# Kernel optimization log

Measured on AMD Instinct MI355X. Metric: run time of the kernel, lower is better.

Reference implementation:

```python
import jax, jax.numpy as jnp
import numpy as np

HIDDEN = 2048
N_HEADS = 16
N_KV = 8
HEAD_DIM = HIDDEN // N_HEADS  # 128
EPS = 1e-6


def rms_norm(x, w, eps=EPS):
    xf = x.astype(jnp.float32)
    var = jnp.mean(xf * xf, axis=-1, keepdims=True)
    return (w * (xf * jax.lax.rsqrt(var + eps)).astype(x.dtype))


def rotate_half(x):
    x1, x2 = jnp.split(x, 2, axis=-1)
    return jnp.concatenate([-x2, x1], axis=-1)


def setup_inputs() -> dict:
    key = jax.random.key(0)
    ks = jax.random.split(key, 8)
    B, S = 2, 2048
    inp = {
        "hidden_states": jax.random.normal(ks[0], (B, S, HIDDEN), jnp.float32),
        "cos": jax.random.uniform(ks[1], (B, S, HEAD_DIM), jnp.float32, -1.0, 1.0),
        "sin": jax.random.uniform(ks[2], (B, S, HEAD_DIM), jnp.float32, -1.0, 1.0),
        "Wq": jax.random.normal(ks[3], (N_HEADS * HEAD_DIM, HIDDEN), jnp.float32) * 0.02,
        "Wk": jax.random.normal(ks[4], (N_KV * HEAD_DIM, HIDDEN), jnp.float32) * 0.02,
        "Wv": jax.random.normal(ks[5], (N_KV * HEAD_DIM, HIDDEN), jnp.float32) * 0.02,
        "Wo": jax.random.normal(ks[6], (HIDDEN, N_HEADS * HEAD_DIM), jnp.float32) * 0.02,
        "q_norm_w": jnp.ones((HEAD_DIM,), jnp.float32),
        "k_norm_w": jnp.ones((HEAD_DIM,), jnp.float32),
    }
    return inp


def reference(hidden_states, cos, sin, Wq, Wk, Wv, Wo, q_norm_w, k_norm_w):
    B, S, _ = hidden_states.shape
    scale = HEAD_DIM ** -0.5
    n_rep = N_HEADS // N_KV

    q = (hidden_states @ Wq.T).reshape(B, S, N_HEADS, HEAD_DIM)
    k = (hidden_states @ Wk.T).reshape(B, S, N_KV, HEAD_DIM)
    v = (hidden_states @ Wv.T).reshape(B, S, N_KV, HEAD_DIM)

    q = rms_norm(q, q_norm_w)
    k = rms_norm(k, k_norm_w)

    # -> (B, H, S, D)
    q = q.transpose(0, 2, 1, 3)
    k = k.transpose(0, 2, 1, 3)
    v = v.transpose(0, 2, 1, 3)

    c = cos[:, None, :, :]  # (B,1,S,D)
    s = sin[:, None, :, :]
    q = q * c + rotate_half(q) * s
    k = k * c + rotate_half(k) * s

    k = jnp.repeat(k, n_rep, axis=1)
    v = jnp.repeat(v, n_rep, axis=1)

    scores = jnp.einsum("bhqd,bhkd->bhqk", q, k) * scale
    attn = jax.nn.softmax(scores.astype(jnp.float32), axis=-1).astype(hidden_states.dtype)
    out = jnp.einsum("bhqk,bhkd->bhqd", attn, v)
    out = out.transpose(0, 2, 1, 3).reshape(B, S, N_HEADS * HEAD_DIM)
    return out @ Wo.T
```

## Files before the change

kernel.cpp:

```cpp
#include <hip/hip_runtime.h>
#include <cstdint>

#define SEQ 2048
#define BATCH 2
#define TOK 4096
#define HID 2048
#define NH 16
#define NKV 8
#define HD 128
#define QKV_LD 4096

using f16x8 = __attribute__((ext_vector_type(8))) _Float16;
using f32x4 = __attribute__((ext_vector_type(4))) float;

#define MFMA(a, b, c) __builtin_amdgcn_mfma_f32_16x16x32_f16(a, b, c, 0, 0, 0)

__device__ inline void gload16(const void* g, void* l) {
    __builtin_amdgcn_global_load_lds(
        (const __attribute__((address_space(1))) unsigned*)g,
        (__attribute__((address_space(3))) unsigned*)l, 16, 0, 0);
}

__device__ inline float exp2_fast(float x) {
#if __has_builtin(__builtin_amdgcn_exp2f)
    return __builtin_amdgcn_exp2f(x);
#else
    float r;
    asm("v_exp_f32 %0, %1\n\ts_nop 1" : "=v"(r) : "v"(x));
    return r;
#endif
}

__device__ inline unsigned cvt_pk2(float a, float b) {
    auto h = __builtin_amdgcn_cvt_pkrtz(a, b);
    return __builtin_bit_cast(unsigned, h);
}

__global__ __launch_bounds__(256) void conv_all(
    const float* __restrict__ hidden, const float* __restrict__ Wq,
    const float* __restrict__ Wk, const float* __restrict__ Wv,
    const float* __restrict__ Wo, _Float16* __restrict__ HhG,
    _Float16* __restrict__ WallH, _Float16* __restrict__ WoH)
{
    const int bid = blockIdx.x;
    const float* src;
    _Float16* dst;
    int row;
    if (bid < 4096)      { row = bid;        src = hidden; dst = HhG; }
    else if (bid < 6144) { row = bid - 4096; src = Wq;     dst = WallH; }
    else if (bid < 7168) { row = bid - 6144; src = Wk;     dst = WallH + (size_t)2048 * HID; }
    else if (bid < 8192) { row = bid - 7168; src = Wv;     dst = WallH + (size_t)3072 * HID; }
    else                 { row = bid - 8192; src = Wo;     dst = WoH; }

    const int gch = threadIdx.x;
    const float* s = src + (size_t)row * HID + gch * 8;
    float4 a = *(const float4*)s;
    float4 b = *(const float4*)(s + 4);
    f16x8 v;
    v[0] = (_Float16)a.x; v[1] = (_Float16)a.y;
    v[2] = (_Float16)a.z; v[3] = (_Float16)a.w;
    v[4] = (_Float16)b.x; v[5] = (_Float16)b.y;
    v[6] = (_Float16)b.z; v[7] = (_Float16)b.w;
    *(f16x8*)((char*)dst + (size_t)row * 4096 + gch * 16) = v;
}

template<bool HALF_OUT>
__global__ __launch_bounds__(512, 2) void gemm256(
    const _Float16* __restrict__ Ag, const _Float16* __restrict__ Bg,
    void* __restrict__ Cv, int ldc, int K)
{
    __shared__ char lds[2][4][16384];

    const int tid = threadIdx.x;
    const int wv = tid >> 6, ln = tid & 63;
    const int wm = wv >> 2, wn = wv & 3;
    const int lr = ln & 15, lq = ln >> 4;
    const int bn = blockIdx.x, bm = blockIdx.y;

    f32x4 acc[8][4] = {};

    const size_t arow0 = (size_t)bm * 256;
    const size_t brow0 = (size_t)bn * 256;

    const int g = tid & 7;
    uint32_t offA[2][2], offB[2][2];
#pragma unroll
    for (int i = 0; i < 2; ++i) {
        const int row = (i * 512 + tid) >> 3;
        const uint32_t sw = (uint32_t)((g ^ (row & 7)) << 4);
        offA[0][i] = (uint32_t)((arow0 + row) * 4096) + sw;
        offA[1][i] = (uint32_t)((arow0 + 128 + row) * 4096) + sw;
        offB[0][i] = (uint32_t)((brow0 + row) * 4096) + sw;
        offB[1][i] = (uint32_t)((brow0 + 128 + row) * 4096) + sw;
    }
    const int dst0 = wv * 64 * 16;

    const int swz0 = ((lq ^ (lr & 7)) << 4);
    const int swz1 = (((4 + lq) ^ (lr & 7)) << 4);

#define STAGE_ALL(bufsel, t)                                                   \
    { _Pragma("unroll")                                                        \
      for (int i = 0; i < 2; ++i) {                                            \
        gload16((const char*)Ag + offA[0][i] + (size_t)(t) * 128,              \
                &lds[bufsel][0][i * 8192 + dst0]);                             \
        gload16((const char*)Ag + offA[1][i] + (size_t)(t) * 128,              \
                &lds[bufsel][1][i * 8192 + dst0]);                             \
        gload16((const char*)Bg + offB[0][i] + (size_t)(t) * 128,              \
                &lds[bufsel][2][i * 8192 + dst0]);                             \
        gload16((const char*)Bg + offB[1][i] + (size_t)(t) * 128,              \
                &lds[bufsel][3][i * 8192 + dst0]);                             \
      } }

    STAGE_ALL(0, 0);
    asm volatile("s_waitcnt vmcnt(0)" ::: "memory");
    __builtin_amdgcn_s_barrier();

    const int NT = K / 64;
    for (int t = 0; t < NT; ++t) {
        const int buf = t & 1;
        const char* Ab = &lds[buf][wm][0];
        const char* Bb = &lds[buf][2 + (wn >> 1)][(wn & 1) * 64 * 128];

        f16x8 bfr[4][2];
#pragma unroll
        for (int nj = 0; nj < 4; ++nj) {
            bfr[nj][0] = *(const f16x8*)(Bb + (nj * 16 + lr) * 128 + swz0);
            bfr[nj][1] = *(const f16x8*)(Bb + (nj * 16 + lr) * 128 + swz1);
        }

        if (t + 1 < NT) STAGE_ALL(buf ^ 1, t + 1);

        __builtin_amdgcn_s_setprio(1);
#pragma unroll
        for (int mi = 0; mi < 8; ++mi) {
            f16x8 a0 = *(const f16x8*)(Ab + (mi * 16 + lr) * 128 + swz0);
            f16x8 a1 = *(const f16x8*)(Ab + (mi * 16 + lr) * 128 + swz1);
#pragma unroll
            for (int nj = 0; nj < 4; ++nj) {
                acc[mi][nj] = MFMA(a0, bfr[nj][0], acc[mi][nj]);
                acc[mi][nj] = MFMA(a1, bfr[nj][1], acc[mi][nj]);
            }
        }
        __builtin_amdgcn_s_setprio(0);

        asm volatile("s_waitcnt vmcnt(0)" ::: "memory");
        __builtin_amdgcn_s_barrier();
    }
#undef STAGE_ALL

#pragma unroll
    for (int mi = 0; mi < 8; ++mi)
#pragma unroll
        for (int r = 0; r < 4; ++r) {
            const size_t rowoff =
                (size_t)(arow0 + wm * 128 + mi * 16 + lq * 4 + r) * ldc
                + brow0 + wn * 64 + lr;
            if constexpr (HALF_OUT) {
                _Float16* rowp = (_Float16*)Cv + rowoff;
#pragma unroll
                for (int nj = 0; nj < 4; ++nj)
                    rowp[nj * 16] = (_Float16)acc[mi][nj][r];
            } else {
                float* rowp = (float*)Cv + rowoff;
#pragma unroll
                for (int nj = 0; nj < 4; ++nj)
                    rowp[nj * 16] = acc[mi][nj][r];
            }
        }
}

__global__ __launch_bounds__(512, 1) void gemm256x128(
    const _Float16* __restrict__ Ag, const _Float16* __restrict__ Bg,
    float* __restrict__ C, int ldc, int K)
{
    __shared__ char lds[2][3][16384];

    const int tid = threadIdx.x;
    const int wv = tid >> 6, ln = tid & 63;
    const int wm = wv >> 1, wn = wv & 1;
    const int lr = ln & 15, lq = ln >> 4;
    const int bn = blockIdx.x, bm = blockIdx.y;

    f32x4 acc[4][4] = {};

    const size_t arow0 = (size_t)bm * 256;
    const size_t brow0 = (size_t)bn * 128;

    const int g = tid & 7;
    uint32_t offA[2][2], offB[2];
#pragma unroll
    for (int i = 0; i < 2; ++i) {
        const int row = (i * 512 + tid) >> 3;
        const uint32_t sw = (uint32_t)((g ^ (row & 7)) << 4);
        offA[0][i] = (uint32_t)((arow0 + row) * 4096) + sw;
        offA[1][i] = (uint32_t)((arow0 + 128 + row) * 4096) + sw;
        offB[i]    = (uint32_t)((brow0 + row) * 4096) + sw;
    }
    const int dst0 = wv * 64 * 16;

    const int swz0 = ((lq ^ (lr & 7)) << 4);
    const int swz1 = (((4 + lq) ^ (lr & 7)) << 4);

#define STAGE_ALL2(bufsel, t)                                                  \
    { _Pragma("unroll")                                                        \
      for (int i = 0; i < 2; ++i) {                                            \
        gload16((const char*)Ag + offA[0][i] + (size_t)(t) * 128,              \
                &lds[bufsel][0][i * 8192 + dst0]);                             \
        gload16((const char*)Ag + offA[1][i] + (size_t)(t) * 128,              \
                &lds[bufsel][1][i * 8192 + dst0]);                             \
        gload16((const char*)Bg + offB[i] + (size_t)(t) * 128,                 \
                &lds[bufsel][2][i * 8192 + dst0]);                             \
      } }

    STAGE_ALL2(0, 0);
    asm volatile("s_waitcnt vmcnt(0)" ::: "memory");
    __builtin_amdgcn_s_barrier();

    const int NT = K / 64;
    for (int t = 0; t < NT; ++t) {
        const int buf = t & 1;
        const char* Ab = &lds[buf][wm >> 1][(wm & 1) * 64 * 128];
        const char* Bb = &lds[buf][2][wn * 64 * 128];

        f16x8 bfr[4][2];
#pragma unroll
        for (int nj = 0; nj < 4; ++nj) {
            bfr[nj][0] = *(const f16x8*)(Bb + (nj * 16 + lr) * 128 + swz0);
            bfr[nj][1] = *(const f16x8*)(Bb + (nj * 16 + lr) * 128 + swz1);
        }

        if (t + 1 < NT) STAGE_ALL2(buf ^ 1, t + 1);

        __builtin_amdgcn_s_setprio(1);
#pragma unroll
        for (int mi = 0; mi < 4; ++mi) {
            f16x8 a0 = *(const f16x8*)(Ab + (mi * 16 + lr) * 128 + swz0);
            f16x8 a1 = *(const f16x8*)(Ab + (mi * 16 + lr) * 128 + swz1);
#pragma unroll
            for (int nj = 0; nj < 4; ++nj) {
                acc[mi][nj] = MFMA(a0, bfr[nj][0], acc[mi][nj]);
                acc[mi][nj] = MFMA(a1, bfr[nj][1], acc[mi][nj]);
            }
        }
        __builtin_amdgcn_s_setprio(0);

        asm volatile("s_waitcnt vmcnt(0)" ::: "memory");
        __builtin_amdgcn_s_barrier();
    }
#undef STAGE_ALL2

#pragma unroll
    for (int mi = 0; mi < 4; ++mi)
#pragma unroll
        for (int r = 0; r < 4; ++r) {
            float* rowp = C + (size_t)(arow0 + wm * 64 + mi * 16 + lq * 4 + r) * ldc
                          + brow0 + wn * 64 + lr;
#pragma unroll
            for (int nj = 0; nj < 4; ++nj)
                rowp[nj * 16] = acc[mi][nj][r];
        }
}

__global__ __launch_bounds__(256) void norm_rope(
    const _Float16* __restrict__ P, const float* __restrict__ cosb,
    const float* __restrict__ sinb, const float* __restrict__ qw,
    const float* __restrict__ kw, _Float16* __restrict__ QhG,
    _Float16* __restrict__ KhG)
{
    const int t    = blockIdx.y;
    const int wave = threadIdx.x >> 6;
    const int lane = threadIdx.x & 63;
    const int hid  = blockIdx.x * 4 + wave;
    const float QS = 0.08838834764831845f * 1.4426950408889634f;

    const _Float16* ptr;
    const float* w;
    if (hid < NH) { ptr = P + (size_t)t * QKV_LD + hid * HD;              w = qw; }
    else          { ptr = P + (size_t)t * QKV_LD + HID + (hid - NH) * HD; w = kw; }

    float x1 = (float)ptr[lane];
    float x2 = (float)ptr[lane + 64];
    float ss = x1 * x1 + x2 * x2;
#pragma unroll
    for (int off = 1; off < 64; off <<= 1) ss += __shfl_xor(ss, off);
    const float r = rsqrtf(ss * (1.f / 128.f) + 1e-6f);
    const float n1 = x1 * r * w[lane];
    const float n2 = x2 * r * w[lane + 64];

    const float* cp = cosb + (size_t)t * HD;
    const float* sp = sinb + (size_t)t * HD;
    const float o1 = n1 * cp[lane]      - n2 * sp[lane];
    const float o2 = n2 * cp[lane + 64] + n1 * sp[lane + 64];

    if (hid < NH) {
        _Float16* qrow = QhG + (size_t)t * HID + hid * HD;
        qrow[lane]      = (_Float16)(o1 * QS);
        qrow[lane + 64] = (_Float16)(o2 * QS);
    } else {
        const int b = t / SEQ, s = t % SEQ, kv = hid - NH;
        char* ph = (char*)KhG + ((size_t)(b * NKV + kv) * SEQ + s) * 256;
        const int s7 = s & 7;
        const int d1 = lane, d2 = lane + 64;
        *(_Float16*)(ph + (((d1 >> 3) ^ s7) << 4) + ((d1 & 7) << 1)) = (_Float16)o1;
        *(_Float16*)(ph + (((d2 >> 3) ^ s7) << 4) + ((d2 & 7) << 1)) = (_Float16)o2;
    }
}

__global__ __launch_bounds__(256) void conv_v(
    const _Float16* __restrict__ P, _Float16* __restrict__ VtG)
{
    __shared__ _Float16 Ts[64][136];
    const int kb = blockIdx.x;
    const int kv = blockIdx.y;
    const int tid = threadIdx.x;

#pragma unroll
    for (int r = 0; r < 4; ++r) {
        const int idx = tid + r * 256;
        const int row = idx >> 4, c8 = idx & 15;
        *(f16x8*)&Ts[row][c8 * 8] =
            *(const f16x8*)(P + (size_t)(kb * 64 + row) * QKV_LD
                            + HID + NKV * HD + kv * HD + c8 * 8);
    }
    __syncthreads();

    const int b  = (kb * 64) / SEQ;
    const int s0 = (kb * 64) % SEQ;
#pragma unroll
    for (int w = 0; w < 4; ++w) {
        const int idx = tid + w * 256;
        const int d = idx >> 3, c = idx & 7;
        f16x8 pk;
#pragma unroll
        for (int kk = 0; kk < 8; ++kk) pk[kk] = Ts[c * 8 + kk][d];
        char* dst = (char*)VtG + ((size_t)(b * NKV + kv) * 128 + d) * 4096
                    + ((s0 >> 3) + (c ^ (d & 7))) * 16;
        *(f16x8*)dst = pk;
    }
}

__global__ __launch_bounds__(256, 2) void flash_f16(
    const _Float16* __restrict__ QhG, const _Float16* __restrict__ KhG,
    const _Float16* __restrict__ VtG, _Float16* __restrict__ OH)
{
    __shared__ char KhL[2][16384];
    __shared__ char VtL[16384];
    __shared__ char PlB[4][5120];

    const int id  = blockIdx.x + 16 * (blockIdx.y + 16 * blockIdx.z);
    const int swz = (id & 7) * 64 + (id >> 3);
    const int qt = swz & 15, h = (swz >> 4) & 15, b = swz >> 8;

    const int hkv = h >> 1;
    const int tid = threadIdx.x, wv = tid >> 6, ln = tid & 63;
    const int lr = ln & 15, lq = ln >> 4;
    const int qbase = qt * 128 + wv * 32;
    const float BIAS = 3.0f * 1.4426950408889634f;

    f16x8 qh[2][4];
#pragma unroll
    for (int mi = 0; mi < 2; ++mi)
#pragma unroll
        for (int kc = 0; kc < 4; ++kc)
            qh[mi][kc] = *(const f16x8*)(QhG
                + (size_t)(b * SEQ + qbase + mi * 16 + lr) * HID
                + h * HD + kc * 32 + lq * 8);

    f32x4 o_[2][8] = {};
    float rs[2] = {0.f, 0.f};

    const size_t krow = (size_t)(b * NKV + hkv) * SEQ;
    const size_t vrow = (size_t)(b * NKV + hkv) * 128;

    const char* kg[4];
    const char* vg[4];
    int dofs[4];
#pragma unroll
    for (int r = 0; r < 4; ++r) {
        const int idx = tid + r * 256;
        kg[r] = (const char*)KhG + (krow + (idx >> 4)) * 256 + (idx & 15) * 16;
        vg[r] = (const char*)VtG + (vrow + (idx >> 3)) * 4096 + (idx & 7) * 16;
        dofs[r] = (r * 256 + wv * 64) * 16;
    }

#define STAGE_K(buf, kt)                                                      \
    { _Pragma("unroll")                                                       \
      for (int r = 0; r < 4; ++r)                                             \
          gload16(kg[r] + (size_t)(kt) * 16384, &KhL[buf][dofs[r]]); }
#define STAGE_V(kt)                                                           \
    { _Pragma("unroll")                                                       \
      for (int r = 0; r < 4; ++r)                                             \
          gload16(vg[r] + (kt) * 128, &VtL[dofs[r]]); }

    STAGE_K(0, 0);
    STAGE_V(0);
    STAGE_K(1, 1);
    __syncthreads();

    const int NT = SEQ / 64;
    for (int kt = 0; kt < NT; ++kt) {
        const int buf = kt & 1;

        f32x4 s[2][4];
        __builtin_amdgcn_s_setprio(1);
#pragma unroll
        for (int nt = 0; nt < 4; ++nt) {
            const int key = nt * 16 + lr;
            f16x8 kh[4];
#pragma unroll
            for (int kc = 0; kc < 4; ++kc)
                kh[kc] = *(f16x8*)(&KhL[buf][key * 256 +
                                   ((((kc * 4 + lq) ^ (lr & 7))) << 4)]);
#pragma unroll
            for (int mi = 0; mi < 2; ++mi) {
                f32x4 sa = {-BIAS, -BIAS, -BIAS, -BIAS};
#pragma unroll
                for (int kc = 0; kc < 4; ++kc)
                    sa = MFMA(kh[kc], qh[mi][kc], sa);
                s[mi][nt] = sa;
            }
        }
        __builtin_amdgcn_s_setprio(0);

#pragma unroll
        for (int mi = 0; mi < 2; ++mi) {
            float acc = 0.f;
            char* rowp = &PlB[wv][(mi * 16 + lr) * 160 + lq * 8];
#pragma unroll
            for (int nt = 0; nt < 4; ++nt) {
                const float p0 = exp2_fast(s[mi][nt][0]);
                const float p1 = exp2_fast(s[mi][nt][1]);
                const float p2 = exp2_fast(s[mi][nt][2]);
                const float p3 = exp2_fast(s[mi][nt][3]);
                acc += (p0 + p1) + (p2 + p3);
                *(uint2*)(rowp + nt * 32) =
                    make_uint2(cvt_pk2(p0, p1), cvt_pk2(p2, p3));
            }
            rs[mi] += acc;
        }
        f16x8 pa[2][2];
#pragma unroll
        for (int mi = 0; mi < 2; ++mi) {
            pa[mi][0] = *(f16x8*)&PlB[wv][(mi * 16 + lr) * 160 + lq * 16];
            pa[mi][1] = *(f16x8*)&PlB[wv][(mi * 16 + lr) * 160 + 64 + lq * 16];
        }

        if (kt + 1 < NT) {
            asm volatile("s_waitcnt vmcnt(4)" ::: "memory");
        } else {
            asm volatile("s_waitcnt vmcnt(0)" ::: "memory");
        }
        __builtin_amdgcn_s_barrier();

        __builtin_amdgcn_s_setprio(1);
#pragma unroll
        for (int nt2 = 0; nt2 < 8; ++nt2) {
            const int d0 = nt2 * 16 + lr;
            f16x8 v0 = *(f16x8*)(&VtL[d0 * 128 + ((lq ^ (d0 & 7)) << 4)]);
            f16x8 v1 = *(f16x8*)(&VtL[d0 * 128 + (((4 + lq) ^ (d0 & 7)) << 4)]);
#pragma unroll
            for (int mi = 0; mi < 2; ++mi) {
                o_[mi][nt2] = MFMA(pa[mi][0], v0, o_[mi][nt2]);
                o_[mi][nt2] = MFMA(pa[mi][1], v1, o_[mi][nt2]);
            }
        }
        __builtin_amdgcn_s_setprio(0);

        __syncthreads();

        if (kt + 1 < NT) STAGE_V(kt + 1);
        if (kt + 2 < NT) STAGE_K(buf, kt + 2);
    }

    float inv[2];
#pragma unroll
    for (int mi = 0; mi < 2; ++mi) {
        float v = rs[mi];
        v += __shfl_xor(v, 16);
        v += __shfl_xor(v, 32);
        inv[mi] = 1.0f / v;
    }
    float invq[2][4];
#pragma unroll
    for (int mi = 0; mi < 2; ++mi)
#pragma unroll
        for (int r = 0; r < 4; ++r)
            invq[mi][r] = __shfl(inv[mi], (ln & 48) | (lq * 4 + r));

#pragma unroll
    for (int mi = 0; mi < 2; ++mi)
#pragma unroll
        for (int r = 0; r < 4; ++r) {
            const int R = b * SEQ + qbase + mi * 16 + lq * 4 + r;
            _Float16* rowp = OH + (size_t)R * HID + h * HD + lr;
#pragma unroll
            for (int nt2 = 0; nt2 < 8; ++nt2)
                rowp[nt2 * 16] = (_Float16)(o_[mi][nt2][r] * invq[mi][r]);
        }
#undef STAGE_K
#undef STAGE_V
}

extern "C" void kernel_launch(void* const* d_in, const int* in_sizes, int n_in,
                              void* d_out, int out_size, void* d_ws, size_t ws_size,
                              hipStream_t stream)
{
    (void)in_sizes; (void)n_in; (void)out_size; (void)ws_size;
    const float* hidden = (const float*)d_in[0];
    const float* cosb   = (const float*)d_in[1];
    const float* sinb   = (const float*)d_in[2];
    const float* Wq     = (const float*)d_in[3];
    const float* Wk     = (const float*)d_in[4];
    const float* Wv     = (const float*)d_in[5];
    const float* Wo     = (const float*)d_in[6];
    const float* qw     = (const float*)d_in[7];
    const float* kw     = (const float*)d_in[8];
    float* out = (float*)d_out;

    char* ws = (char*)d_ws;
    const size_t MB = 1ull << 20;
    _Float16*  P16   = (_Float16*)(ws);
    _Float16*  attnH = (_Float16*)(ws + 32  * MB);
    _Float16*  HhG   = (_Float16*)(ws + 48  * MB);
    _Float16*  WallH = (_Float16*)(ws + 64  * MB);
    _Float16*  WoH   = (_Float16*)(ws + 80  * MB);
    _Float16*  KhG   = (_Float16*)(ws + 88  * MB);
    _Float16*  VtG   = (_Float16*)(ws + 96  * MB);
    _Float16*  QhG   = (_Float16*)(ws + 104 * MB);

    const dim3 blk(256);
    conv_all<<<10240, blk, 0, stream>>>(hidden, Wq, Wk, Wv, Wo, HhG, WallH, WoH);

    gemm256<true><<<dim3(16, 16), dim3(512), 0, stream>>>(HhG, WallH, P16, QKV_LD, HID);

    norm_rope<<<dim3(6, TOK), blk, 0, stream>>>(P16, cosb, sinb, qw, kw, QhG, KhG);
    conv_v<<<dim3(TOK / 64, NKV), blk, 0, stream>>>(P16, VtG);

    flash_f16<<<dim3(SEQ / 128, NH, BATCH), blk, 0, stream>>>(QhG, KhG, VtG, attnH);

    gemm256x128<<<dim3(16, 16), dim3(512), 0, stream>>>(attnH, WoH, out, HID, HID);
}
```

Measured before the change: 213.2 us.

## Deepen GEMM global-to-LDS pipeline to prefetch two tiles ahead

```diff
diff --git a/kernel.cpp b/kernel.cpp
--- a/kernel.cpp
+++ b/kernel.cpp
@@ -112,7 +112,8 @@
       } }
 
     STAGE_ALL(0, 0);
-    asm volatile("s_waitcnt vmcnt(0)" ::: "memory");
+    STAGE_ALL(1, 1);
+    asm volatile("s_waitcnt vmcnt(8)" ::: "memory");
     __builtin_amdgcn_s_barrier();
 
     const int NT = K / 64;
@@ -121,29 +122,37 @@
         const char* Ab = &lds[buf][wm][0];
         const char* Bb = &lds[buf][2 + (wn >> 1)][(wn & 1) * 64 * 128];
 
-        f16x8 bfr[4][2];
+        f16x8 bfr[4][2], afr[8][2];
 #pragma unroll
         for (int nj = 0; nj < 4; ++nj) {
             bfr[nj][0] = *(const f16x8*)(Bb + (nj * 16 + lr) * 128 + swz0);
             bfr[nj][1] = *(const f16x8*)(Bb + (nj * 16 + lr) * 128 + swz1);
         }
-
-        if (t + 1 < NT) STAGE_ALL(buf ^ 1, t + 1);
+#pragma unroll
+        for (int mi = 0; mi < 8; ++mi) {
+            afr[mi][0] = *(const f16x8*)(Ab + (mi * 16 + lr) * 128 + swz0);
+            afr[mi][1] = *(const f16x8*)(Ab + (mi * 16 + lr) * 128 + swz1);
+        }
+        asm volatile("s_waitcnt lgkmcnt(0)" ::: "memory");
+        __builtin_amdgcn_s_barrier();
+
+        if (t + 2 < NT) STAGE_ALL(buf, t + 2);
 
         __builtin_amdgcn_s_setprio(1);
 #pragma unroll
-        for (int mi = 0; mi < 8; ++mi) {
-            f16x8 a0 = *(const f16x8*)(Ab + (mi * 16 + lr) * 128 + swz0);
-            f16x8 a1 = *(const f16x8*)(Ab + (mi * 16 + lr) * 128 + swz1);
+        for (int mi = 0; mi < 8; ++mi)
 #pragma unroll
             for (int nj = 0; nj < 4; ++nj) {
-                acc[mi][nj] = MFMA(a0, bfr[nj][0], acc[mi][nj]);
-                acc[mi][nj] = MFMA(a1, bfr[nj][1], acc[mi][nj]);
+                acc[mi][nj] = MFMA(afr[mi][0], bfr[nj][0], acc[mi][nj]);
+                acc[mi][nj] = MFMA(afr[mi][1], bfr[nj][1], acc[mi][nj]);
             }
-        }
         __builtin_amdgcn_s_setprio(0);
 
-        asm volatile("s_waitcnt vmcnt(0)" ::: "memory");
+        if (t + 2 < NT) {
+            asm volatile("s_waitcnt vmcnt(8)" ::: "memory");
+        } else {
+            asm volatile("s_waitcnt vmcnt(0)" ::: "memory");
+        }
         __builtin_amdgcn_s_barrier();
     }
 #undef STAGE_ALL
@@ -213,7 +222,8 @@
       } }
 
     STAGE_ALL2(0, 0);
-    asm volatile("s_waitcnt vmcnt(0)" ::: "memory");
+    STAGE_ALL2(1, 1);
+    asm volatile("s_waitcnt vmcnt(6)" ::: "memory");
     __builtin_amdgcn_s_barrier();
 
     const int NT = K / 64;
@@ -222,29 +232,37 @@
         const char* Ab = &lds[buf][wm >> 1][(wm & 1) * 64 * 128];
         const char* Bb = &lds[buf][2][wn * 64 * 128];
 
-        f16x8 bfr[4][2];
+        f16x8 bfr[4][2], afr[4][2];
 #pragma unroll
         for (int nj = 0; nj < 4; ++nj) {
             bfr[nj][0] = *(const f16x8*)(Bb + (nj * 16 + lr) * 128 + swz0);
             bfr[nj][1] = *(const f16x8*)(Bb + (nj * 16 + lr) * 128 + swz1);
         }
-
-        if (t + 1 < NT) STAGE_ALL2(buf ^ 1, t + 1);
+#pragma unroll
+        for (int mi = 0; mi < 4; ++mi) {
+            afr[mi][0] = *(const f16x8*)(Ab + (mi * 16 + lr) * 128 + swz0);
+            afr[mi][1] = *(const f16x8*)(Ab + (mi * 16 + lr) * 128 + swz1);
+        }
+        asm volatile("s_waitcnt lgkmcnt(0)" ::: "memory");
+        __builtin_amdgcn_s_barrier();
+
+        if (t + 2 < NT) STAGE_ALL2(buf, t + 2);
 
         __builtin_amdgcn_s_setprio(1);
 #pragma unroll
-        for (int mi = 0; mi < 4; ++mi) {
-            f16x8 a0 = *(const f16x8*)(Ab + (mi * 16 + lr) * 128 + swz0);
-            f16x8 a1 = *(const f16x8*)(Ab + (mi * 16 + lr) * 128 + swz1);
+        for (int mi = 0; mi < 4; ++mi)
 #pragma unroll
             for (int nj = 0; nj < 4; ++nj) {
-                acc[mi][nj] = MFMA(a0, bfr[nj][0], acc[mi][nj]);
-                acc[mi][nj] = MFMA(a1, bfr[nj][1], acc[mi][nj]);
+                acc[mi][nj] = MFMA(afr[mi][0], bfr[nj][0], acc[mi][nj]);
+                acc[mi][nj] = MFMA(afr[mi][1], bfr[nj][1], acc[mi][nj]);
             }
-        }
         __builtin_amdgcn_s_setprio(0);
 
-        asm volatile("s_waitcnt vmcnt(0)" ::: "memory");
+        if (t + 2 < NT) {
+            asm volatile("s_waitcnt vmcnt(6)" ::: "memory");
+        } else {
+            asm volatile("s_waitcnt vmcnt(0)" ::: "memory");
+        }
         __builtin_amdgcn_s_barrier();
     }
 #undef STAGE_ALL2
```

Result: slower. 219.6 us (+3.0%).
